# Kernel tuning notes

Hardware: AMD Instinct MI355X
Metric: run time of the kernel (lower is better)

The kernel has to match this reference:

```python
import jax, jax.numpy as jnp
import numpy as np

N, IN_DIM, HIDDEN, NUM_CLASSES, K = 4096, 1024, 128, 10, 2
N_EDGES = 65536


def setup_inputs() -> dict:
    key = jax.random.key(0)
    k0, k1, k2, k3 = jax.random.split(key, 4)
    X = jax.random.normal(k0, (N, IN_DIM), dtype=jnp.float32)
    edge_index = jax.random.randint(k1, (2, N_EDGES), 0, N, dtype=jnp.int64)
    W_embed = jax.random.normal(k2, (IN_DIM, HIDDEN), dtype=jnp.float32) / np.sqrt(IN_DIM)
    b_embed = jnp.zeros((HIDDEN,), dtype=jnp.float32)
    final_dim = (2 ** (K + 1) - 1) * HIDDEN  # 896
    W_cls = jax.random.normal(k3, (final_dim, NUM_CLASSES), dtype=jnp.float32) / np.sqrt(final_dim)
    b_cls = jnp.zeros((NUM_CLASSES,), dtype=jnp.float32)
    return {"X": X, "edge_index": edge_index, "W_embed": W_embed,
            "b_embed": b_embed, "W_cls": W_cls, "b_cls": b_cls}


def _normalize(A):
    # symmetric normalization D^{-1/2} A D^{-1/2}, expressed with broadcasting
    deg = A.sum(axis=1)
    d_inv_sqrt = (deg + 1e-8) ** -0.5
    return d_inv_sqrt[:, None] * A * d_inv_sqrt[None, :]


def reference(X, edge_index, W_embed, b_embed, W_cls, b_cls):
    n = X.shape[0]
    # dense adjacency from edge list (matches torch A[src, dst] = 1)
    A = jnp.zeros((n, n), dtype=X.dtype).at[edge_index[0], edge_index[1]].set(1.0)
    A1 = _normalize(A)
    # clean 2-hop adjacency: (A@A - A - I) > 0, then normalized
    A2 = A @ A - A - jnp.eye(n, dtype=X.dtype)
    A2 = _normalize((A2 > 0).astype(X.dtype))
    # embed (dropout is identity in eval)
    r = jax.nn.relu(X @ W_embed + b_embed)
    reps = [r]
    for _ in range(K):
        r = jnp.concatenate([A1 @ r, A2 @ r], axis=1)
        reps.append(r)
    r_final = jnp.concatenate(reps, axis=1)  # [n, (2^(K+1)-1)*hidden]
    return r_final @ W_cls + b_cls
```

## Files before the change

### kernel.cpp

```cpp
#include <hip/hip_runtime.h>
#include <hip/hip_bf16.h>
#include <stdint.h>

#define NN      4096
#define IN_DIM  1024
#define HID     128
#define RF      896
#define NW      128
#define CAP1    64
#define CAP2    1024
#define KS      8
#define KC      (IN_DIM/KS)

typedef __attribute__((ext_vector_type(8))) short   bf16x8;
typedef __attribute__((ext_vector_type(4))) float   f32x4;
typedef __attribute__((ext_vector_type(2))) float   f32x2;

static __device__ __forceinline__ uint16_t f2bf(float f) {
    __hip_bfloat16 h = __float2bfloat16(f);
    return *reinterpret_cast<uint16_t*>(&h);
}
static __device__ __forceinline__ float bf2f(uint16_t u) {
    __hip_bfloat16 h = *reinterpret_cast<__hip_bfloat16*>(&u);
    return __bfloat162float(h);
}
static __device__ __forceinline__ uint32_t packbf(float lo, float hi) {
    return (uint32_t)f2bf(lo) | ((uint32_t)f2bf(hi) << 16);
}
template<int HI>
static __device__ __forceinline__ uint32_t pk8(float a, float b, uint32_t old) {
    return __builtin_amdgcn_cvt_pk_fp8_f32(a, b, old, HI);
}
template<int HI>
static __device__ __forceinline__ f32x2 upk8(uint32_t u) {
    return __builtin_amdgcn_cvt_pk_f32_fp8(u, HI);
}

__global__ __launch_bounds__(256) void prep(
    uint32_t* __restrict__ Abits, uint32_t* __restrict__ p10, uint32_t* __restrict__ p20,
    uint32_t* __restrict__ p11, uint32_t* __restrict__ p21,
    const float* __restrict__ W, uint16_t* __restrict__ Wt_hi, uint16_t* __restrict__ Wt_lo)
{
    int b = blockIdx.x, t = threadIdx.x;
    if (b < 512) {
        reinterpret_cast<uint4*>(Abits)[b * 256 + t] = make_uint4(0, 0, 0, 0);
    } else if (b == 512) {
        if (t < 32) { p10[(size_t)NN * 32 + t] = 0; p20[(size_t)NN * 32 + t] = 0; }
        if (t < 64) { p11[(size_t)NN * 64 + t] = 0; p21[(size_t)NN * 64 + t] = 0; }
    } else {
        if (t < 128) {
            int n  = t;
            int k0 = (b - 513) * 8;
            uint16_t h[8], l[8];
            #pragma unroll
            for (int j = 0; j < 8; ++j) {
                float x = W[(size_t)(k0 + j) * HID + n];
                h[j] = f2bf(x);
                l[j] = f2bf(x - bf2f(h[j]));
            }
            ushort4* ph = reinterpret_cast<ushort4*>(Wt_hi + (size_t)n * IN_DIM + k0);
            ushort4* pl = reinterpret_cast<ushort4*>(Wt_lo + (size_t)n * IN_DIM + k0);
            ph[0] = make_ushort4(h[0], h[1], h[2], h[3]);
            ph[1] = make_ushort4(h[4], h[5], h[6], h[7]);
            pl[0] = make_ushort4(l[0], l[1], l[2], l[3]);
            pl[1] = make_ushort4(l[4], l[5], l[6], l[7]);
        }
    }
}

__global__ void scatter_edges(const int* __restrict__ ei, uint32_t* __restrict__ Abits, int nE) {
    int e = blockIdx.x * blockDim.x + threadIdx.x;
    if (e < nE) {
        int s = ei[e];
        int d = ei[nE + e];
        atomicOr(&Abits[(size_t)s * NW + (d >> 5)], 1u << (d & 31));
    }
}

#define UPD(v) { s3x |= s2x & (v).x; s2x |= s1x & (v).x; s1x |= (v).x; \
                 s3y |= s2y & (v).y; s2y |= s1y & (v).y; s1y |= (v).y; }
__global__ __launch_bounds__(256) void twohop2(
    const uint32_t* __restrict__ Abits,
    uint16_t* __restrict__ adj1, uint16_t* __restrict__ adj2,
    int* __restrict__ deg1p, int* __restrict__ deg2p,
    float* __restrict__ d1, float* __restrict__ d2)
{
    __shared__ uint16_t l1s[4][CAP1];

    int wv = threadIdx.x >> 6, lane = threadIdx.x & 63;
    int i = blockIdx.x * 4 + wv;

    uint2 sv = *reinterpret_cast<const uint2*>(&Abits[(size_t)i * NW + lane * 2]);

    int pc1 = __popc(sv.x) + __popc(sv.y);
    int x1 = pc1;
    #pragma unroll
    for (int off = 1; off < 64; off <<= 1) {
        int y = __shfl_up(x1, off);
        if (lane >= off) x1 += y;
    }
    int tot1 = __shfl(x1, 63);
    int o = x1 - pc1;
    {
        uint32_t b = sv.x;
        while (b) { int bb = __ffs(b) - 1; b &= b - 1;
                    uint16_t v = (uint16_t)(lane * 64 + bb);
                    l1s[wv][o] = v; adj1[(size_t)i * CAP1 + o] = v; ++o; }
        b = sv.y;
        while (b) { int bb = __ffs(b) - 1; b &= b - 1;
                    uint16_t v = (uint16_t)(lane * 64 + 32 + bb);
                    l1s[wv][o] = v; adj1[(size_t)i * CAP1 + o] = v; ++o; }
    }
    int n1 = (tot1 + 3) & ~3;
    if (lane == 0) {
        for (int z = tot1; z < n1; ++z) adj1[(size_t)i * CAP1 + z] = (uint16_t)NN;
        deg1p[i] = n1;
        d1[i] = rsqrtf((float)tot1 + 1e-8f);
    }
    __syncthreads();

    uint32_t s1x = 0, s2x = 0, s3x = 0, s1y = 0, s2y = 0, s3y = 0;
    int m = 0;
    for (; m + 4 <= tot1; m += 4) {
        int k0 = l1s[wv][m], k1 = l1s[wv][m + 1], k2 = l1s[wv][m + 2], k3 = l1s[wv][m + 3];
        uint2 a = *reinterpret_cast<const uint2*>(&Abits[(size_t)k0 * NW + lane * 2]);
        uint2 b = *reinterpret_cast<const uint2*>(&Abits[(size_t)k1 * NW + lane * 2]);
        uint2 c = *reinterpret_cast<const uint2*>(&Abits[(size_t)k2 * NW + lane * 2]);
        uint2 d = *reinterpret_cast<const uint2*>(&Abits[(size_t)k3 * NW + lane * 2]);
        UPD(a); UPD(b); UPD(c); UPD(d);
    }
    for (; m < tot1; ++m) {
        int k = l1s[wv][m];
        uint2 a = *reinterpret_cast<const uint2*>(&Abits[(size_t)k * NW + lane * 2]);
        UPD(a);
    }

    uint32_t iwx = ((i >> 5) == lane * 2)     ? (1u << (i & 31)) : 0u;
    uint32_t iwy = ((i >> 5) == lane * 2 + 1) ? (1u << (i & 31)) : 0u;
    uint32_t a2x = (s1x & ~sv.x & ~iwx) | (s2x & (sv.x ^ iwx)) | (s3x & (sv.x & iwx));
    uint32_t a2y = (s1y & ~sv.y & ~iwy) | (s2y & (sv.y ^ iwy)) | (s3y & (sv.y & iwy));

    int pc2 = __popc(a2x) + __popc(a2y);
    int x2 = pc2;
    #pragma unroll
    for (int off = 1; off < 64; off <<= 1) {
        int y = __shfl_up(x2, off);
        if (lane >= off) x2 += y;
    }
    int tot2 = __shfl(x2, 63);
    o = x2 - pc2;
    {
        uint32_t b = a2x;
        while (b) { int bb = __ffs(b) - 1; b &= b - 1;
                    adj2[(size_t)i * CAP2 + o] = (uint16_t)(lane * 64 + bb); ++o; }
        b = a2y;
        while (b) { int bb = __ffs(b) - 1; b &= b - 1;
                    adj2[(size_t)i * CAP2 + o] = (uint16_t)(lane * 64 + 32 + bb); ++o; }
    }
    int n2 = (tot2 + 3) & ~3;
    if (lane == 0) {
        for (int z = tot2; z < n2; ++z) adj2[(size_t)i * CAP2 + z] = (uint16_t)NN;
        deg2p[i] = n2;
        d2[i] = rsqrtf((float)tot2 + 1e-8f);
    }
}

#define XSTR 136
__global__ __launch_bounds__(128) void embed_mfma(
    const float* __restrict__ X, const uint16_t* __restrict__ Wt_hi,
    const uint16_t* __restrict__ Wt_lo, float* __restrict__ partials)
{
    __shared__ uint16_t XhiS[32][XSTR];
    __shared__ uint16_t XloS[32][XSTR];
    __shared__ uint16_t WS[128][XSTR];

    int t  = threadIdx.x;
    int m0 = blockIdx.x * 32;
    int kc = blockIdx.y;

    #pragma unroll
    for (int u = 0; u < 8; ++u) {
        int q = u * 128 + t;
        int row = q >> 5, c4 = q & 31;
        float4 xv = *reinterpret_cast<const float4*>(
            X + (size_t)(m0 + row) * IN_DIM + kc * KC + c4 * 4);
        ushort4 hv, lv;
        hv.x = f2bf(xv.x); lv.x = f2bf(xv.x - bf2f(hv.x));
        hv.y = f2bf(xv.y); lv.y = f2bf(xv.y - bf2f(hv.y));
        hv.z = f2bf(xv.z); lv.z = f2bf(xv.z - bf2f(hv.z));
        hv.w = f2bf(xv.w); lv.w = f2bf(xv.w - bf2f(hv.w));
        *reinterpret_cast<ushort4*>(&XhiS[row][c4 * 4]) = hv;
        *reinterpret_cast<ushort4*>(&XloS[row][c4 * 4]) = lv;
    }
    #pragma unroll
    for (int u = 0; u < 16; ++u) {
        int q = u * 128 + t;
        int n = q >> 4, ck = q & 15;
        *reinterpret_cast<uint4*>(&WS[n][ck * 8]) =
            *reinterpret_cast<const uint4*>(Wt_hi + (size_t)n * IN_DIM + kc * KC + ck * 8);
    }
    __syncthreads();

    int w = t >> 6, lane = t & 63;
    int nr = lane & 15, g = lane >> 4;
    int arow = w * 16 + nr;

    bf16x8 ah[4], al[4];
    #pragma unroll
    for (int s = 0; s < 4; ++s) {
        ah[s] = *reinterpret_cast<const bf16x8*>(&XhiS[arow][s * 32 + g * 8]);
        al[s] = *reinterpret_cast<const bf16x8*>(&XloS[arow][s * 32 + g * 8]);
    }

    f32x4 acc[8] = {};

    #pragma unroll
    for (int s = 0; s < 4; ++s)
        #pragma unroll
        for (int nf = 0; nf < 8; ++nf) {
            bf16x8 bb = *reinterpret_cast<const bf16x8*>(&WS[nf * 16 + nr][s * 32 + g * 8]);
            acc[nf] = __builtin_amdgcn_mfma_f32_16x16x32_bf16(ah[s], bb, acc[nf], 0, 0, 0);
            acc[nf] = __builtin_amdgcn_mfma_f32_16x16x32_bf16(al[s], bb, acc[nf], 0, 0, 0);
        }
    __syncthreads();
    #pragma unroll
    for (int u = 0; u < 16; ++u) {
        int q = u * 128 + t;
        int n = q >> 4, ck = q & 15;
        *reinterpret_cast<uint4*>(&WS[n][ck * 8]) =
            *reinterpret_cast<const uint4*>(Wt_lo + (size_t)n * IN_DIM + kc * KC + ck * 8);
    }
    __syncthreads();
    #pragma unroll
    for (int s = 0; s < 4; ++s)
        #pragma unroll
        for (int nf = 0; nf < 8; ++nf) {
            bf16x8 bb = *reinterpret_cast<const bf16x8*>(&WS[nf * 16 + nr][s * 32 + g * 8]);
            acc[nf] = __builtin_amdgcn_mfma_f32_16x16x32_bf16(ah[s], bb, acc[nf], 0, 0, 0);
        }

    float* part = partials + (size_t)kc * NN * HID;
    #pragma unroll
    for (int nf = 0; nf < 8; ++nf)
        #pragma unroll
        for (int r = 0; r < 4; ++r)
            part[(size_t)(m0 + w * 16 + g * 4 + r) * HID + nf * 16 + nr] = acc[nf][r];
}

__global__ void embed_reduce(const float* __restrict__ partials, const float* __restrict__ bias,
                             const float* __restrict__ d1, const float* __restrict__ d2,
                             uint16_t* __restrict__ rfb, uint32_t* __restrict__ P1,
                             uint32_t* __restrict__ P2) {
    int idx = blockIdx.x * blockDim.x + threadIdx.x;
    size_t off = (size_t)idx * 4;
    int row = (int)(off >> 7);
    int col = (int)(off & 127);

    float4 s = make_float4(0.f, 0.f, 0.f, 0.f);
    #pragma unroll
    for (int kc = 0; kc < KS; ++kc) {
        float4 p = *reinterpret_cast<const float4*>(partials + (size_t)kc * NN * HID + off);
        s.x += p.x; s.y += p.y; s.z += p.z; s.w += p.w;
    }
    float4 bv = *reinterpret_cast<const float4*>(bias + col);
    float4 v;
    v.x = fmaxf(s.x + bv.x, 0.f);
    v.y = fmaxf(s.y + bv.y, 0.f);
    v.z = fmaxf(s.z + bv.z, 0.f);
    v.w = fmaxf(s.w + bv.w, 0.f);

    uint2 rv;
    rv.x = packbf(v.x, v.y); rv.y = packbf(v.z, v.w);
    *reinterpret_cast<uint2*>(rfb + (size_t)row * RF + col) = rv;

    float s1 = d1[row], s2 = d2[row];
    uint32_t w1 = pk8<0>(s1 * v.x, s1 * v.y, 0u);
    w1 = pk8<1>(s1 * v.z, s1 * v.w, w1);
    P1[(size_t)row * 32 + (col >> 2)] = w1;
    uint32_t w2 = pk8<0>(s2 * v.x, s2 * v.y, 0u);
    w2 = pk8<1>(s2 * v.z, s2 * v.w, w2);
    P2[(size_t)row * 32 + (col >> 2)] = w2;
}

__global__ __launch_bounds__(256) void gather_k1(
    const uint16_t* __restrict__ adj1, const uint16_t* __restrict__ adj2,
    const int* __restrict__ deg1p, const int* __restrict__ deg2p,
    const uint32_t* __restrict__ P10, const uint32_t* __restrict__ P20,
    const float* __restrict__ d1, const float* __restrict__ d2,
    uint16_t* __restrict__ rfb, uint32_t* __restrict__ P11, uint32_t* __restrict__ P21)
{
    int lane = threadIdx.x & 63;
    int gw   = __builtin_amdgcn_readfirstlane((blockIdx.x * 256 + threadIdx.x) >> 6);
    int i    = gw >> 1;
    int mat  = gw & 1;
    int nb = lane >> 4, cq = lane & 15;
    int shamt = lane & 48;

    const uint16_t* adj = mat ? adj2 + (size_t)i * CAP2 : adj1 + (size_t)i * CAP1;
    int n = (mat ? deg2p : deg1p)[i];
    const uint32_t* P = mat ? P20 : P10;

    f32x2 acc[4] = {};
    #pragma unroll 8
    for (int m = 0; m < n; m += 4) {
        uint64_t aw = *reinterpret_cast<const uint64_t*>(adj + m);
        int j = (int)((uint32_t)(aw >> shamt) & 0xffffu);
        uint2 u = *reinterpret_cast<const uint2*>(P + (size_t)j * 32 + cq * 2);
        acc[0] += upk8<0>(u.x);
        acc[1] += upk8<1>(u.x);
        acc[2] += upk8<0>(u.y);
        acc[3] += upk8<1>(u.y);
    }
    #pragma unroll
    for (int k = 0; k < 4; ++k) {
        acc[k].x += __shfl_xor(acc[k].x, 16); acc[k].y += __shfl_xor(acc[k].y, 16);
        acc[k].x += __shfl_xor(acc[k].x, 32); acc[k].y += __shfl_xor(acc[k].y, 32);
    }

    if (nb == 0) {
        float di = (mat ? d2 : d1)[i];
        float o[8];
        #pragma unroll
        for (int k = 0; k < 4; ++k) { o[2 * k] = di * acc[k].x; o[2 * k + 1] = di * acc[k].y; }

        uint4 rv;
        rv.x = packbf(o[0], o[1]); rv.y = packbf(o[2], o[3]);
        rv.z = packbf(o[4], o[5]); rv.w = packbf(o[6], o[7]);
        *reinterpret_cast<uint4*>(rfb + (size_t)i * RF + 128 + mat * 128 + cq * 8) = rv;

        float s1 = d1[i], s2 = d2[i];
        uint2 v1, v2;
        v1.x = pk8<0>(s1 * o[0], s1 * o[1], 0u);
        v1.x = pk8<1>(s1 * o[2], s1 * o[3], v1.x);
        v1.y = pk8<0>(s1 * o[4], s1 * o[5], 0u);
        v1.y = pk8<1>(s1 * o[6], s1 * o[7], v1.y);
        v2.x = pk8<0>(s2 * o[0], s2 * o[1], 0u);
        v2.x = pk8<1>(s2 * o[2], s2 * o[3], v2.x);
        v2.y = pk8<0>(s2 * o[4], s2 * o[5], 0u);
        v2.y = pk8<1>(s2 * o[6], s2 * o[7], v2.y);
        *reinterpret_cast<uint2*>(P11 + (size_t)i * 64 + mat * 32 + cq * 2) = v1;
        *reinterpret_cast<uint2*>(P21 + (size_t)i * 64 + mat * 32 + cq * 2) = v2;
    }
}

__global__ __launch_bounds__(256) void gather_k2(
    const uint16_t* __restrict__ adj1, const uint16_t* __restrict__ adj2,
    const int* __restrict__ deg1p, const int* __restrict__ deg2p,
    const uint32_t* __restrict__ P11, const uint32_t* __restrict__ P21,
    const float* __restrict__ d1, const float* __restrict__ d2,
    uint16_t* __restrict__ rfb)
{
    int wv   = threadIdx.x >> 6;
    int lane = threadIdx.x & 63;
    int seg  = blockIdx.x >> 10;
    int i    = __builtin_amdgcn_readfirstlane((blockIdx.x & 1023) * 4 + wv);
    int mat  = seg >> 1;
    int half = seg & 1;
    int nb = lane >> 4, cq = lane & 15;
    int shamt = lane & 48;

    const uint16_t* adj = mat ? adj2 + (size_t)i * CAP2 : adj1 + (size_t)i * CAP1;
    int n = (mat ? deg2p : deg1p)[i];
    const uint32_t* P = (mat ? P21 : P11) + half * 32 + cq * 2;

    f32x2 acc[4] = {};
    #pragma unroll 8
    for (int m = 0; m < n; m += 4) {
        uint64_t aw = *reinterpret_cast<const uint64_t*>(adj + m);
        int j = (int)((uint32_t)(aw >> shamt) & 0xffffu);
        uint2 u = *reinterpret_cast<const uint2*>(P + (size_t)j * 64);
        acc[0] += upk8<0>(u.x);
        acc[1] += upk8<1>(u.x);
        acc[2] += upk8<0>(u.y);
        acc[3] += upk8<1>(u.y);
    }
    #pragma unroll
    for (int k = 0; k < 4; ++k) {
        acc[k].x += __shfl_xor(acc[k].x, 16); acc[k].y += __shfl_xor(acc[k].y, 16);
        acc[k].x += __shfl_xor(acc[k].x, 32); acc[k].y += __shfl_xor(acc[k].y, 32);
    }

    if (nb == 0) {
        float di = (mat ? d2 : d1)[i];
        int colbase = 384 + mat * 256 + half * 128 + cq * 8;
        uint4 rv;
        rv.x = packbf(di * acc[0].x, di * acc[0].y);
        rv.y = packbf(di * acc[1].x, di * acc[1].y);
        rv.z = packbf(di * acc[2].x, di * acc[2].y);
        rv.w = packbf(di * acc[3].x, di * acc[3].y);
        *reinterpret_cast<uint4*>(rfb + (size_t)i * RF + colbase) = rv;
    }
}

__global__ __launch_bounds__(256) void cls_bf(
    const uint16_t* __restrict__ rfb, const float* __restrict__ Wc,
    const float* __restrict__ bc, float* __restrict__ out)
{
    int wave = threadIdx.x >> 6;
    int lane = threadIdx.x & 63;
    int row  = blockIdx.x * 4 + wave;

    const uint32_t* rp = reinterpret_cast<const uint32_t*>(rfb + (size_t)row * RF);
    float acc[10] = {};
    #pragma unroll
    for (int k7 = 0; k7 < 7; ++k7) {
        int k = k7 * 64 + lane;
        uint32_t u = rp[k];
        float x0 = __uint_as_float(u << 16);
        float x1 = __uint_as_float(u & 0xffff0000u);
        const float* w = Wc + (size_t)k * 20;
        #pragma unroll
        for (int c = 0; c < 10; ++c) acc[c] += x0 * w[c] + x1 * w[10 + c];
    }
    #pragma unroll
    for (int c = 0; c < 10; ++c)
        #pragma unroll
        for (int off = 32; off; off >>= 1) acc[c] += __shfl_down(acc[c], off);

    if (lane == 0) {
        #pragma unroll
        for (int c = 0; c < 10; ++c) out[(size_t)row * 10 + c] = acc[c] + bc[c];
    }
}

extern "C" void kernel_launch(void* const* d_in, const int* in_sizes, int n_in,
                              void* d_out, int out_size, void* d_ws, size_t ws_size,
                              hipStream_t stream) {
    const float* X       = (const float*)d_in[0];
    const int*   ei      = (const int*)d_in[1];
    const float* W_embed = (const float*)d_in[2];
    const float* b_embed = (const float*)d_in[3];
    const float* W_cls   = (const float*)d_in[4];
    const float* b_cls   = (const float*)d_in[5];
    float* out = (float*)d_out;

    int nE = in_sizes[1] / 2;

    uint32_t* Abits = (uint32_t*)d_ws;
    float* d1 = (float*)(Abits + (size_t)NN * NW);
    float* d2 = d1 + NN;
    uint16_t* rfb = (uint16_t*)(d2 + NN);
    uint32_t* P1_0 = (uint32_t*)(rfb + (size_t)NN * RF);
    uint32_t* P2_0 = P1_0 + (size_t)(NN + 1) * 32;
    uint32_t* P1_1 = P2_0 + (size_t)(NN + 1) * 32;
    uint32_t* P2_1 = P1_1 + (size_t)(NN + 1) * 64;
    uint16_t* Wt_hi = (uint16_t*)(P2_1 + (size_t)(NN + 1) * 64);
    uint16_t* Wt_lo = Wt_hi + (size_t)HID * IN_DIM;
    float* partials = (float*)(Wt_lo + (size_t)HID * IN_DIM);
    uint16_t* adj1 = (uint16_t*)(partials + (size_t)KS * NN * HID);
    uint16_t* adj2 = adj1 + (size_t)NN * CAP1;
    int* deg1p = (int*)(adj2 + (size_t)NN * CAP2);
    int* deg2p = deg1p + NN;

    prep<<<641, 256, 0, stream>>>(Abits, P1_0, P2_0, P1_1, P2_1,
                                  W_embed, Wt_hi, Wt_lo);
    scatter_edges<<<(nE + 255) / 256, 256, 0, stream>>>(ei, Abits, nE);
    twohop2<<<NN / 4, 256, 0, stream>>>(Abits, adj1, adj2, deg1p, deg2p, d1, d2);

    embed_mfma<<<dim3(NN / 32, KS), 128, 0, stream>>>(X, Wt_hi, Wt_lo, partials);
    embed_reduce<<<(NN * HID / 4) / 256, 256, 0, stream>>>(partials, b_embed, d1, d2,
                                                           rfb, P1_0, P2_0);

    gather_k1<<<NN * 2 * 64 / 256, 256, 0, stream>>>(
        adj1, adj2, deg1p, deg2p, P1_0, P2_0, d1, d2, rfb, P1_1, P2_1);
    gather_k2<<<NN * 4 * 64 / 256, 256, 0, stream>>>(
        adj1, adj2, deg1p, deg2p, P1_1, P2_1, d1, d2, rfb);

    cls_bf<<<NN / 4, 256, 0, stream>>>(rfb, W_cls, b_cls, out);
}
```

Baseline: 85.68 us.

## Merge two-hop adjacency build and embedding MFMA into one interleaved launch

```diff
diff --git a/kernel.cpp b/kernel.cpp
--- a/kernel.cpp
+++ b/kernel.cpp
@@ -11,6 +11,7 @@
 #define CAP2    1024
 #define KS      8
 #define KC      (IN_DIM/KS)
+#define XSTR    136
 
 typedef __attribute__((ext_vector_type(8))) short   bf16x8;
 typedef __attribute__((ext_vector_type(4))) float   f32x4;
@@ -79,172 +80,176 @@
 
 #define UPD(v) { s3x |= s2x & (v).x; s2x |= s1x & (v).x; s1x |= (v).x; \
                  s3y |= s2y & (v).y; s2y |= s1y & (v).y; s1y |= (v).y; }
-__global__ __launch_bounds__(256) void twohop2(
+__global__ __launch_bounds__(256) void build_embed(
     const uint32_t* __restrict__ Abits,
     uint16_t* __restrict__ adj1, uint16_t* __restrict__ adj2,
     int* __restrict__ deg1p, int* __restrict__ deg2p,
-    float* __restrict__ d1, float* __restrict__ d2)
-{
-    __shared__ uint16_t l1s[4][CAP1];
-
-    int wv = threadIdx.x >> 6, lane = threadIdx.x & 63;
-    int i = blockIdx.x * 4 + wv;
-
-    uint2 sv = *reinterpret_cast<const uint2*>(&Abits[(size_t)i * NW + lane * 2]);
-
-    int pc1 = __popc(sv.x) + __popc(sv.y);
-    int x1 = pc1;
-    #pragma unroll
-    for (int off = 1; off < 64; off <<= 1) {
-        int y = __shfl_up(x1, off);
-        if (lane >= off) x1 += y;
-    }
-    int tot1 = __shfl(x1, 63);
-    int o = x1 - pc1;
-    {
-        uint32_t b = sv.x;
-        while (b) { int bb = __ffs(b) - 1; b &= b - 1;
-                    uint16_t v = (uint16_t)(lane * 64 + bb);
-                    l1s[wv][o] = v; adj1[(size_t)i * CAP1 + o] = v; ++o; }
-        b = sv.y;
-        while (b) { int bb = __ffs(b) - 1; b &= b - 1;
-                    uint16_t v = (uint16_t)(lane * 64 + 32 + bb);
-                    l1s[wv][o] = v; adj1[(size_t)i * CAP1 + o] = v; ++o; }
-    }
-    int n1 = (tot1 + 3) & ~3;
-    if (lane == 0) {
-        for (int z = tot1; z < n1; ++z) adj1[(size_t)i * CAP1 + z] = (uint16_t)NN;
-        deg1p[i] = n1;
-        d1[i] = rsqrtf((float)tot1 + 1e-8f);
-    }
-    __syncthreads();
-
-    uint32_t s1x = 0, s2x = 0, s3x = 0, s1y = 0, s2y = 0, s3y = 0;
-    int m = 0;
-    for (; m + 4 <= tot1; m += 4) {
-        int k0 = l1s[wv][m], k1 = l1s[wv][m + 1], k2 = l1s[wv][m + 2], k3 = l1s[wv][m + 3];
-        uint2 a = *reinterpret_cast<const uint2*>(&Abits[(size_t)k0 * NW + lane * 2]);
-        uint2 b = *reinterpret_cast<const uint2*>(&Abits[(size_t)k1 * NW + lane * 2]);
-        uint2 c = *reinterpret_cast<const uint2*>(&Abits[(size_t)k2 * NW + lane * 2]);
-        uint2 d = *reinterpret_cast<const uint2*>(&Abits[(size_t)k3 * NW + lane * 2]);
-        UPD(a); UPD(b); UPD(c); UPD(d);
-    }
-    for (; m < tot1; ++m) {
-        int k = l1s[wv][m];
-        uint2 a = *reinterpret_cast<const uint2*>(&Abits[(size_t)k * NW + lane * 2]);
-        UPD(a);
-    }
-
-    uint32_t iwx = ((i >> 5) == lane * 2)     ? (1u << (i & 31)) : 0u;
-    uint32_t iwy = ((i >> 5) == lane * 2 + 1) ? (1u << (i & 31)) : 0u;
-    uint32_t a2x = (s1x & ~sv.x & ~iwx) | (s2x & (sv.x ^ iwx)) | (s3x & (sv.x & iwx));
-    uint32_t a2y = (s1y & ~sv.y & ~iwy) | (s2y & (sv.y ^ iwy)) | (s3y & (sv.y & iwy));
-
-    int pc2 = __popc(a2x) + __popc(a2y);
-    int x2 = pc2;
-    #pragma unroll
-    for (int off = 1; off < 64; off <<= 1) {
-        int y = __shfl_up(x2, off);
-        if (lane >= off) x2 += y;
-    }
-    int tot2 = __shfl(x2, 63);
-    o = x2 - pc2;
-    {
-        uint32_t b = a2x;
-        while (b) { int bb = __ffs(b) - 1; b &= b - 1;
-                    adj2[(size_t)i * CAP2 + o] = (uint16_t)(lane * 64 + bb); ++o; }
-        b = a2y;
-        while (b) { int bb = __ffs(b) - 1; b &= b - 1;
-                    adj2[(size_t)i * CAP2 + o] = (uint16_t)(lane * 64 + 32 + bb); ++o; }
-    }
-    int n2 = (tot2 + 3) & ~3;
-    if (lane == 0) {
-        for (int z = tot2; z < n2; ++z) adj2[(size_t)i * CAP2 + z] = (uint16_t)NN;
-        deg2p[i] = n2;
-        d2[i] = rsqrtf((float)tot2 + 1e-8f);
-    }
-}
-
-#define XSTR 136
-__global__ __launch_bounds__(128) void embed_mfma(
+    float* __restrict__ d1, float* __restrict__ d2,
     const float* __restrict__ X, const uint16_t* __restrict__ Wt_hi,
     const uint16_t* __restrict__ Wt_lo, float* __restrict__ partials)
 {
-    __shared__ uint16_t XhiS[32][XSTR];
-    __shared__ uint16_t XloS[32][XSTR];
-    __shared__ uint16_t WS[128][XSTR];
-
-    int t  = threadIdx.x;
-    int m0 = blockIdx.x * 32;
-    int kc = blockIdx.y;
-
-    #pragma unroll
-    for (int u = 0; u < 8; ++u) {
-        int q = u * 128 + t;
-        int row = q >> 5, c4 = q & 31;
-        float4 xv = *reinterpret_cast<const float4*>(
-            X + (size_t)(m0 + row) * IN_DIM + kc * KC + c4 * 4);
-        ushort4 hv, lv;
-        hv.x = f2bf(xv.x); lv.x = f2bf(xv.x - bf2f(hv.x));
-        hv.y = f2bf(xv.y); lv.y = f2bf(xv.y - bf2f(hv.y));
-        hv.z = f2bf(xv.z); lv.z = f2bf(xv.z - bf2f(hv.z));
-        hv.w = f2bf(xv.w); lv.w = f2bf(xv.w - bf2f(hv.w));
-        *reinterpret_cast<ushort4*>(&XhiS[row][c4 * 4]) = hv;
-        *reinterpret_cast<ushort4*>(&XloS[row][c4 * 4]) = lv;
-    }
-    #pragma unroll
-    for (int u = 0; u < 16; ++u) {
-        int q = u * 128 + t;
-        int n = q >> 4, ck = q & 15;
-        *reinterpret_cast<uint4*>(&WS[n][ck * 8]) =
-            *reinterpret_cast<const uint4*>(Wt_hi + (size_t)n * IN_DIM + kc * KC + ck * 8);
-    }
-    __syncthreads();
-
-    int w = t >> 6, lane = t & 63;
-    int nr = lane & 15, g = lane >> 4;
-    int arow = w * 16 + nr;
-
-    bf16x8 ah[4], al[4];
-    #pragma unroll
-    for (int s = 0; s < 4; ++s) {
-        ah[s] = *reinterpret_cast<const bf16x8*>(&XhiS[arow][s * 32 + g * 8]);
-        al[s] = *reinterpret_cast<const bf16x8*>(&XloS[arow][s * 32 + g * 8]);
-    }
-
-    f32x4 acc[8] = {};
-
-    #pragma unroll
-    for (int s = 0; s < 4; ++s)
-        #pragma unroll
-        for (int nf = 0; nf < 8; ++nf) {
-            bf16x8 bb = *reinterpret_cast<const bf16x8*>(&WS[nf * 16 + nr][s * 32 + g * 8]);
-            acc[nf] = __builtin_amdgcn_mfma_f32_16x16x32_bf16(ah[s], bb, acc[nf], 0, 0, 0);
-            acc[nf] = __builtin_amdgcn_mfma_f32_16x16x32_bf16(al[s], bb, acc[nf], 0, 0, 0);
-        }
-    __syncthreads();
-    #pragma unroll
-    for (int u = 0; u < 16; ++u) {
-        int q = u * 128 + t;
-        int n = q >> 4, ck = q & 15;
-        *reinterpret_cast<uint4*>(&WS[n][ck * 8]) =
-            *reinterpret_cast<const uint4*>(Wt_lo + (size_t)n * IN_DIM + kc * KC + ck * 8);
-    }
-    __syncthreads();
-    #pragma unroll
-    for (int s = 0; s < 4; ++s)
-        #pragma unroll
-        for (int nf = 0; nf < 8; ++nf) {
-            bf16x8 bb = *reinterpret_cast<const bf16x8*>(&WS[nf * 16 + nr][s * 32 + g * 8]);
-            acc[nf] = __builtin_amdgcn_mfma_f32_16x16x32_bf16(ah[s], bb, acc[nf], 0, 0, 0);
-        }
-
-    float* part = partials + (size_t)kc * NN * HID;
-    #pragma unroll
-    for (int nf = 0; nf < 8; ++nf)
-        #pragma unroll
-        for (int r = 0; r < 4; ++r)
-            part[(size_t)(m0 + w * 16 + g * 4 + r) * HID + nf * 16 + nr] = acc[nf][r];
+    __shared__ __align__(16) uint16_t smem[192 * XSTR];
+
+    int b = blockIdx.x, t = threadIdx.x;
+
+    if ((b & 1) == 0) {
+        uint16_t (*l1s)[CAP1] = reinterpret_cast<uint16_t(*)[CAP1]>(smem);
+        int h = b >> 1;
+        int wv = t >> 6, lane = t & 63;
+        int i = h * 4 + wv;
+
+        uint2 sv = *reinterpret_cast<const uint2*>(&Abits[(size_t)i * NW + lane * 2]);
+
+        int pc1 = __popc(sv.x) + __popc(sv.y);
+        int x1 = pc1;
+        #pragma unroll
+        for (int off = 1; off < 64; off <<= 1) {
+            int y = __shfl_up(x1, off);
+            if (lane >= off) x1 += y;
+        }
+        int tot1 = __shfl(x1, 63);
+        int o = x1 - pc1;
+        {
+            uint32_t bb_ = sv.x;
+            while (bb_) { int bb = __ffs(bb_) - 1; bb_ &= bb_ - 1;
+                          uint16_t v = (uint16_t)(lane * 64 + bb);
+                          l1s[wv][o] = v; adj1[(size_t)i * CAP1 + o] = v; ++o; }
+            bb_ = sv.y;
+            while (bb_) { int bb = __ffs(bb_) - 1; bb_ &= bb_ - 1;
+                          uint16_t v = (uint16_t)(lane * 64 + 32 + bb);
+                          l1s[wv][o] = v; adj1[(size_t)i * CAP1 + o] = v; ++o; }
+        }
+        int n1 = (tot1 + 3) & ~3;
+        if (lane == 0) {
+            for (int z = tot1; z < n1; ++z) adj1[(size_t)i * CAP1 + z] = (uint16_t)NN;
+            deg1p[i] = n1;
+            d1[i] = rsqrtf((float)tot1 + 1e-8f);
+        }
+        __syncthreads();
+
+        uint32_t s1x = 0, s2x = 0, s3x = 0, s1y = 0, s2y = 0, s3y = 0;
+        int m = 0;
+        for (; m + 4 <= tot1; m += 4) {
+            int k0 = l1s[wv][m], k1 = l1s[wv][m + 1], k2 = l1s[wv][m + 2], k3 = l1s[wv][m + 3];
+            uint2 a = *reinterpret_cast<const uint2*>(&Abits[(size_t)k0 * NW + lane * 2]);
+            uint2 bq = *reinterpret_cast<const uint2*>(&Abits[(size_t)k1 * NW + lane * 2]);
+            uint2 c = *reinterpret_cast<const uint2*>(&Abits[(size_t)k2 * NW + lane * 2]);
+            uint2 d = *reinterpret_cast<const uint2*>(&Abits[(size_t)k3 * NW + lane * 2]);
+            UPD(a); UPD(bq); UPD(c); UPD(d);
+        }
+        for (; m < tot1; ++m) {
+            int k = l1s[wv][m];
+            uint2 a = *reinterpret_cast<const uint2*>(&Abits[(size_t)k * NW + lane * 2]);
+            UPD(a);
+        }
+
+        uint32_t iwx = ((i >> 5) == lane * 2)     ? (1u << (i & 31)) : 0u;
+        uint32_t iwy = ((i >> 5) == lane * 2 + 1) ? (1u << (i & 31)) : 0u;
+        uint32_t a2x = (s1x & ~sv.x & ~iwx) | (s2x & (sv.x ^ iwx)) | (s3x & (sv.x & iwx));
+        uint32_t a2y = (s1y & ~sv.y & ~iwy) | (s2y & (sv.y ^ iwy)) | (s3y & (sv.y & iwy));
+
+        int pc2 = __popc(a2x) + __popc(a2y);
+        int x2 = pc2;
+        #pragma unroll
+        for (int off = 1; off < 64; off <<= 1) {
+            int y = __shfl_up(x2, off);
+            if (lane >= off) x2 += y;
+        }
+        int tot2 = __shfl(x2, 63);
+        o = x2 - pc2;
+        {
+            uint32_t bb_ = a2x;
+            while (bb_) { int bb = __ffs(bb_) - 1; bb_ &= bb_ - 1;
+                          adj2[(size_t)i * CAP2 + o] = (uint16_t)(lane * 64 + bb); ++o; }
+            bb_ = a2y;
+            while (bb_) { int bb = __ffs(bb_) - 1; bb_ &= bb_ - 1;
+                          adj2[(size_t)i * CAP2 + o] = (uint16_t)(lane * 64 + 32 + bb); ++o; }
+        }
+        int n2 = (tot2 + 3) & ~3;
+        if (lane == 0) {
+            for (int z = tot2; z < n2; ++z) adj2[(size_t)i * CAP2 + z] = (uint16_t)NN;
+            deg2p[i] = n2;
+            d2[i] = rsqrtf((float)tot2 + 1e-8f);
+        }
+    } else {
+        uint16_t (*XhiS)[XSTR] = reinterpret_cast<uint16_t(*)[XSTR]>(smem);
+        uint16_t (*XloS)[XSTR] = reinterpret_cast<uint16_t(*)[XSTR]>(smem + 32 * XSTR);
+        uint16_t (*WS)[XSTR]   = reinterpret_cast<uint16_t(*)[XSTR]>(smem + 64 * XSTR);
+
+        int e  = b >> 1;
+        int m0 = (e & 127) * 32;
+        int kc = e >> 7;
+
+        #pragma unroll
+        for (int u = 0; u < 4; ++u) {
+            int q = u * 256 + t;
+            int row = q >> 5, c4 = q & 31;
+            float4 xv = *reinterpret_cast<const float4*>(
+                X + (size_t)(m0 + row) * IN_DIM + kc * KC + c4 * 4);
+            ushort4 hv, lv;
+            hv.x = f2bf(xv.x); lv.x = f2bf(xv.x - bf2f(hv.x));
+            hv.y = f2bf(xv.y); lv.y = f2bf(xv.y - bf2f(hv.y));
+            hv.z = f2bf(xv.z); lv.z = f2bf(xv.z - bf2f(hv.z));
+            hv.w = f2bf(xv.w); lv.w = f2bf(xv.w - bf2f(hv.w));
+            *reinterpret_cast<ushort4*>(&XhiS[row][c4 * 4]) = hv;
+            *reinterpret_cast<ushort4*>(&XloS[row][c4 * 4]) = lv;
+        }
+        #pragma unroll
+        for (int u = 0; u < 8; ++u) {
+            int q = u * 256 + t;
+            int n = q >> 4, ck = q & 15;
+            *reinterpret_cast<uint4*>(&WS[n][ck * 8]) =
+                *reinterpret_cast<const uint4*>(Wt_hi + (size_t)n * IN_DIM + kc * KC + ck * 8);
+        }
+        __syncthreads();
+
+        int w = t >> 6, lane = t & 63;
+        int nr = lane & 15, g = lane >> 4;
+        f32x4 acc[8] = {};
+        bf16x8 ah[4], al[4];
+
+        if (t < 128) {
+            int arow = w * 16 + nr;
+            #pragma unroll
+            for (int s = 0; s < 4; ++s) {
+                ah[s] = *reinterpret_cast<const bf16x8*>(&XhiS[arow][s * 32 + g * 8]);
+                al[s] = *reinterpret_cast<const bf16x8*>(&XloS[arow][s * 32 + g * 8]);
+            }
+            #pragma unroll
+            for (int s = 0; s < 4; ++s)
+                #pragma unroll
+                for (int nf = 0; nf < 8; ++nf) {
+                    bf16x8 bb = *reinterpret_cast<const bf16x8*>(&WS[nf * 16 + nr][s * 32 + g * 8]);
+                    acc[nf] = __builtin_amdgcn_mfma_f32_16x16x32_bf16(ah[s], bb, acc[nf], 0, 0, 0);
+                    acc[nf] = __builtin_amdgcn_mfma_f32_16x16x32_bf16(al[s], bb, acc[nf], 0, 0, 0);
+                }
+        }
+        __syncthreads();
+        #pragma unroll
+        for (int u = 0; u < 8; ++u) {
+            int q = u * 256 + t;
+            int n = q >> 4, ck = q & 15;
+            *reinterpret_cast<uint4*>(&WS[n][ck * 8]) =
+                *reinterpret_cast<const uint4*>(Wt_lo + (size_t)n * IN_DIM + kc * KC + ck * 8);
+        }
+        __syncthreads();
+        if (t < 128) {
+            #pragma unroll
+            for (int s = 0; s < 4; ++s)
+                #pragma unroll
+                for (int nf = 0; nf < 8; ++nf) {
+                    bf16x8 bb = *reinterpret_cast<const bf16x8*>(&WS[nf * 16 + nr][s * 32 + g * 8]);
+                    acc[nf] = __builtin_amdgcn_mfma_f32_16x16x32_bf16(ah[s], bb, acc[nf], 0, 0, 0);
+                }
+
+            float* part = partials + (size_t)kc * NN * HID;
+            #pragma unroll
+            for (int nf = 0; nf < 8; ++nf)
+                #pragma unroll
+                for (int r = 0; r < 4; ++r)
+                    part[(size_t)(m0 + w * 16 + g * 4 + r) * HID + nf * 16 + nr] = acc[nf][r];
+        }
+    }
 }
 
 __global__ void embed_reduce(const float* __restrict__ partials, const float* __restrict__ bias,
@@ -455,9 +460,10 @@
     prep<<<641, 256, 0, stream>>>(Abits, P1_0, P2_0, P1_1, P2_1,
                                   W_embed, Wt_hi, Wt_lo);
     scatter_edges<<<(nE + 255) / 256, 256, 0, stream>>>(ei, Abits, nE);
-    twohop2<<<NN / 4, 256, 0, stream>>>(Abits, adj1, adj2, deg1p, deg2p, d1, d2);
-
-    embed_mfma<<<dim3(NN / 32, KS), 128, 0, stream>>>(X, Wt_hi, Wt_lo, partials);
+
+    build_embed<<<2048, 256, 0, stream>>>(Abits, adj1, adj2, deg1p, deg2p, d1, d2,
+                                          X, Wt_hi, Wt_lo, partials);
+
     embed_reduce<<<(NN * HID / 4) / 256, 256, 0, stream>>>(partials, b_embed, d1, d2,
                                                            rfb, P1_0, P2_0);
 
```

Result: no change. 85.94 us (+0.3%).
